# Performance work log

Hardware: AMD Instinct MI355X
Metric: run time of the kernel (lower is better)

## Reference

```python
import jax, jax.numpy as jnp
import numpy as np

B, D_IN = 4096, 32000
H0, H1, TAIL = 4000, 4000, 2000
SPARSITY = 0.98


def setup_inputs() -> dict:
    key = jax.random.key(0)
    ks = jax.random.split(key, 8)
    vals = jax.random.normal(ks[0], (B, D_IN), dtype=jnp.float32)
    mask = jax.random.uniform(ks[1], (B, D_IN)) > SPARSITY
    X = vals * mask.astype(jnp.float32)
    def xavier(k, fan_in, fan_out):
        gain = jnp.sqrt(2.0)  # calculate_gain('relu')
        bound = gain * jnp.sqrt(6.0 / (fan_in + fan_out))
        return jax.random.uniform(k, (fan_in, fan_out), dtype=jnp.float32,
                                  minval=-bound, maxval=bound)
    return {
        'X': X,
        'W_in': xavier(ks[2], D_IN, H0), 'b_in': jnp.full((H0,), 0.1, jnp.float32),
        'W1': xavier(ks[3], H0, H1),     'b1': jnp.full((H1,), 0.1, jnp.float32),
        'W2': xavier(ks[4], H1, TAIL),   'b2': jnp.full((TAIL,), 0.1, jnp.float32),
    }


def reference(X, W_in, b_in, W1, b1, W2, b2):
    # SparseLinear: sparse-dense mm + bias (here expressed as dense mm)
    out = jnp.dot(X, W_in) + b_in            # [B, H0]
    # block 0: Linear -> ReLU (dropout identity at eval)
    out = jax.nn.relu(jnp.dot(out, W1) + b1)  # [B, H1]
    # block 1 (tail): Linear -> ReLU
    out = jax.nn.relu(jnp.dot(out, W2) + b2)  # [B, TAIL]
    return out
```

## Files before the change

### kernel.cpp

```cpp
#include <hip/hip_runtime.h>
#include <stdint.h>
#include <stddef.h>


typedef __attribute__((ext_vector_type(8))) short short8;
typedef __attribute__((ext_vector_type(4))) float f32x4;
typedef __attribute__((ext_vector_type(4))) uint32_t u32x4;
typedef __attribute__((ext_vector_type(2))) uint32_t u32x2;

__device__ __forceinline__ uint32_t f2bf_bits(float f) {
  uint32_t u = __builtin_bit_cast(uint32_t, f);
  u += 0x7FFFu + ((u >> 16) & 1u);
  return u >> 16;
}
__device__ __forceinline__ uint32_t pk2(float a, float b) {
  return f2bf_bits(a) | (f2bf_bits(b) << 16);
}

__device__ __forceinline__ void gload_lds16(const uint16_t* g, uint16_t* l) {
  __builtin_amdgcn_global_load_lds(
      (const __attribute__((address_space(1))) uint32_t*)g,
      (__attribute__((address_space(3))) uint32_t*)l, 16, 0, 0);
}

__global__ __launch_bounds__(256)
void cvt_bf16_kernel(const float* __restrict__ in, uint32_t* __restrict__ out, size_t n) {
  size_t i = ((size_t)blockIdx.x * 256 + threadIdx.x) * 8;
  if (i + 8 <= n) {
    f32x4 a = *(const f32x4*)(in + i);
    f32x4 b = *(const f32x4*)(in + i + 4);
    u32x4 o = {pk2(a.x, a.y), pk2(a.z, a.w), pk2(b.x, b.y), pk2(b.z, b.w)};
    *(u32x4*)(out + i / 2) = o;
  }
}

__global__ __launch_bounds__(256)
void cvtT_bf16_kernel(const float* __restrict__ in, uint16_t* __restrict__ out, int K, int N) {
  __shared__ float tile[32][33];
  const int kb = blockIdx.y * 32;
  const int nb = blockIdx.x * 32;
  const int tx = threadIdx.x & 31;
  const int ty = threadIdx.x >> 5;
  const int ncol = nb + tx;
#pragma unroll
  for (int i = 0; i < 32; i += 8)
    tile[ty + i][tx] = (ncol < N) ? in[(size_t)(kb + ty + i) * N + ncol] : 0.f;
  __syncthreads();
#pragma unroll
  for (int i = 0; i < 32; i += 8) {
    int nrow = nb + ty + i;
    if (nrow < N)
      out[(size_t)nrow * K + (kb + tx)] = (uint16_t)f2bf_bits(tile[tx][ty + i]);
  }
}

template<bool RELU, bool OBF16>
__global__ __launch_bounds__(256, 2)
void mlp_gemm_fast(const uint16_t* __restrict__ A, const uint16_t* __restrict__ Bt,
                   const float* __restrict__ bias, void* __restrict__ Cp,
                   int M, int N, int K)
{
  __shared__ uint16_t As[128 * 32];
  __shared__ uint16_t Bs[128 * 32];

  const int tid  = threadIdx.x;
  const int lane = tid & 63;
  const int wave = __builtin_amdgcn_readfirstlane(tid >> 6);

  const int gx = gridDim.x;
  int nwg = gx * (int)gridDim.y;
  int wg = (int)blockIdx.y * gx + (int)blockIdx.x;
  if ((nwg & 7) == 0) { int c = nwg >> 3; wg = (wg & 7) * c + (wg >> 3); }
  const int n0 = (wg % gx) << 7;
  const int m0 = (wg / gx) << 7;

  const int wm = (wave & 1) << 6;
  const int wn = (wave >> 1) << 6;
  const int fl = lane & 15;
  const int kg = lane >> 4;

  const int sr = lane >> 2;
  const int sp = lane & 3;
  const int r0 = wave * 32 + sr;
  const int ssw = ((sp ^ ((r0 >> 1) & 3)) << 3);

  const uint16_t* gA0 = A + (size_t)(m0 + r0) * K + ssw;
  const uint16_t* gA1 = gA0 + (size_t)16 * K;
  int bn0 = n0 + r0;      if (bn0 > N - 1) bn0 = N - 1;
  int bn1 = n0 + r0 + 16; if (bn1 > N - 1) bn1 = N - 1;
  const uint16_t* gB0 = Bt + (size_t)bn0 * K + ssw;
  const uint16_t* gB1 = Bt + (size_t)bn1 * K + ssw;

  uint16_t* lA0 = &As[wave * 1024];
  uint16_t* lA1 = lA0 + 512;
  uint16_t* lB0 = &Bs[wave * 1024];
  uint16_t* lB1 = lB0 + 512;

  const int colsw = ((kg ^ ((fl >> 1) & 3)) << 3);

  f32x4 acc[4][4];
#pragma unroll
  for (int i = 0; i < 4; ++i)
#pragma unroll
    for (int j = 0; j < 4; ++j)
      acc[i][j] = f32x4{0.f, 0.f, 0.f, 0.f};

  for (int k0 = 0; k0 < K; k0 += 32) {
    gload_lds16(gA0, lA0);
    gload_lds16(gA1, lA1);
    gload_lds16(gB0, lB0);
    gload_lds16(gB1, lB1);
    gA0 += 32; gA1 += 32; gB0 += 32; gB1 += 32;
    __syncthreads();

    short8 af[4], bfr[4];
#pragma unroll
    for (int t = 0; t < 4; ++t) {
      af[t]  = *(const short8*)&As[(wm + t * 16 + fl) * 32 + colsw];
      bfr[t] = *(const short8*)&Bs[(wn + t * 16 + fl) * 32 + colsw];
    }
#pragma unroll
    for (int tm = 0; tm < 4; ++tm)
#pragma unroll
      for (int tn = 0; tn < 4; ++tn)
        acc[tm][tn] = __builtin_amdgcn_mfma_f32_16x16x32_bf16(af[tm], bfr[tn], acc[tm][tn], 0, 0, 0);
    __syncthreads();
  }

#pragma unroll
  for (int tn = 0; tn < 4; ++tn) {
    int n = n0 + wn + tn * 16 + fl;
    if (n < N) {
      float bv = bias[n];
#pragma unroll
      for (int tm = 0; tm < 4; ++tm) {
        size_t base = (size_t)(m0 + wm + tm * 16 + kg * 4) * N + n;
#pragma unroll
        for (int r = 0; r < 4; ++r) {
          float v = acc[tm][tn][r] + bv;
          if constexpr (RELU) v = fmaxf(v, 0.f);
          if constexpr (OBF16)
            ((uint16_t*)Cp)[base + (size_t)r * N] = (uint16_t)f2bf_bits(v);
          else
            ((float*)Cp)[base + (size_t)r * N] = v;
        }
      }
    }
  }
}

template<bool ABF16, bool BTBF16, bool RELU, bool OBF16>
__global__ __launch_bounds__(256, 2)
void mlp_gemm(const void* __restrict__ Ap, const void* __restrict__ Bp,
              const float* __restrict__ bias, void* __restrict__ Cp,
              int M, int N, int K)
{
  __shared__ uint16_t As[128][40];
  __shared__ uint16_t Bs[128][40];

  const int tid  = threadIdx.x;
  const int lane = tid & 63;
  const int wave = tid >> 6;
  const int wm = (wave & 1) << 6;
  const int wn = (wave >> 1) << 6;
  const int fl = lane & 15;
  const int kg = lane >> 4;

  const int m0 = blockIdx.y << 7;
  const int n0 = blockIdx.x << 7;

  const int ar = tid >> 1;
  const int ah = (tid & 1) << 4;
  const int bkb = tid >> 5;
  const int bnb = tid & 31;

  const bool n_full = (n0 + 128 <= N);
  const int brow = (n0 + ar < N) ? (n0 + ar) : (N - 1);

  f32x4 acc[4][4];
#pragma unroll
  for (int i = 0; i < 4; ++i)
#pragma unroll
    for (int j = 0; j < 4; ++j)
      acc[i][j] = f32x4{0.f, 0.f, 0.f, 0.f};

  for (int k0 = 0; k0 < K; k0 += 32) {
    {
      u32x4 w0, w1;
      if constexpr (ABF16) {
        const uint16_t* A = (const uint16_t*)Ap;
        const uint16_t* p = A + (size_t)(m0 + ar) * K + (k0 + ah);
        w0 = ((const u32x4*)p)[0];
        w1 = ((const u32x4*)p)[1];
      } else {
        const float* A = (const float*)Ap;
        const float* p = A + (size_t)(m0 + ar) * K + (k0 + ah);
        f32x4 a0 = ((const f32x4*)p)[0];
        f32x4 a1 = ((const f32x4*)p)[1];
        f32x4 a2 = ((const f32x4*)p)[2];
        f32x4 a3 = ((const f32x4*)p)[3];
        w0 = u32x4{pk2(a0.x, a0.y), pk2(a0.z, a0.w), pk2(a1.x, a1.y), pk2(a1.z, a1.w)};
        w1 = u32x4{pk2(a2.x, a2.y), pk2(a2.z, a2.w), pk2(a3.x, a3.y), pk2(a3.z, a3.w)};
      }
      u32x4* d = (u32x4*)&As[ar][ah];
      d[0] = w0; d[1] = w1;
    }
    if constexpr (BTBF16) {
      const uint16_t* Bt = (const uint16_t*)Bp;
      const uint16_t* p = Bt + (size_t)brow * K + (k0 + ah);
      u32x4 w0 = ((const u32x4*)p)[0];
      u32x4 w1 = ((const u32x4*)p)[1];
      u32x4* d = (u32x4*)&Bs[ar][ah];
      d[0] = w0; d[1] = w1;
    } else {
      const float* Bmat = (const float*)Bp;
      if (n_full) {
        const float* p = Bmat + (size_t)(k0 + bkb * 4) * N + (n0 + bnb * 4);
        f32x4 r0 = *(const f32x4*)p;
        f32x4 r1 = *(const f32x4*)(p + (size_t)N);
        f32x4 r2 = *(const f32x4*)(p + 2 * (size_t)N);
        f32x4 r3 = *(const f32x4*)(p + 3 * (size_t)N);
#pragma unroll
        for (int ii = 0; ii < 4; ++ii) {
          u32x2 w = {pk2(r0[ii], r1[ii]), pk2(r2[ii], r3[ii])};
          *(u32x2*)&Bs[bnb * 4 + ii][bkb * 4] = w;
        }
      } else {
#pragma unroll
        for (int ii = 0; ii < 4; ++ii) {
          int n = n0 + bnb * 4 + ii;
          uint32_t b0 = 0, b1 = 0, b2 = 0, b3 = 0;
          if (n < N) {
            size_t o = (size_t)(k0 + bkb * 4) * N + n;
            b0 = f2bf_bits(Bmat[o]);
            b1 = f2bf_bits(Bmat[o + (size_t)N]);
            b2 = f2bf_bits(Bmat[o + 2 * (size_t)N]);
            b3 = f2bf_bits(Bmat[o + 3 * (size_t)N]);
          }
          u32x2 w = {b0 | (b1 << 16), b2 | (b3 << 16)};
          *(u32x2*)&Bs[bnb * 4 + ii][bkb * 4] = w;
        }
      }
    }
    __syncthreads();

    short8 af[4], bfr[4];
#pragma unroll
    for (int t = 0; t < 4; ++t) {
      af[t]  = *(const short8*)&As[wm + t * 16 + fl][kg * 8];
      bfr[t] = *(const short8*)&Bs[wn + t * 16 + fl][kg * 8];
    }
#pragma unroll
    for (int tm = 0; tm < 4; ++tm)
#pragma unroll
      for (int tn = 0; tn < 4; ++tn)
        acc[tm][tn] = __builtin_amdgcn_mfma_f32_16x16x32_bf16(af[tm], bfr[tn], acc[tm][tn], 0, 0, 0);
    __syncthreads();
  }

#pragma unroll
  for (int tn = 0; tn < 4; ++tn) {
    int n = n0 + wn + tn * 16 + fl;
    if (n < N) {
      float bv = bias[n];
#pragma unroll
      for (int tm = 0; tm < 4; ++tm) {
        size_t base = (size_t)(m0 + wm + tm * 16 + kg * 4) * N + n;
#pragma unroll
        for (int r = 0; r < 4; ++r) {
          float v = acc[tm][tn][r] + bv;
          if constexpr (RELU) v = fmaxf(v, 0.f);
          if constexpr (OBF16)
            ((uint16_t*)Cp)[base + (size_t)r * N] = (uint16_t)f2bf_bits(v);
          else
            ((float*)Cp)[base + (size_t)r * N] = v;
        }
      }
    }
  }
}

extern "C" void kernel_launch(void* const* d_in, const int* in_sizes, int n_in,
                              void* d_out, int out_size, void* d_ws, size_t ws_size,
                              hipStream_t stream) {
  const float* X   = (const float*)d_in[0];
  const float* Win = (const float*)d_in[1];
  const float* bin = (const float*)d_in[2];
  const float* W1  = (const float*)d_in[3];
  const float* b1  = (const float*)d_in[4];
  const float* W2  = (const float*)d_in[5];
  const float* b2  = (const float*)d_in[6];
  float* out = (float*)d_out;

  const int Bm = 4096, DIN = 32000, H0 = 4000, H1 = 4000, TL = 2000;
  const size_t sX  = (size_t)Bm * DIN;
  const size_t sWi = (size_t)DIN * H0;
  const size_t sW1 = (size_t)H0 * H1;
  const size_t sW2 = (size_t)H1 * TL;
  const size_t st0 = (size_t)Bm * H0;
  const size_t st1 = (size_t)Bm * H1;
  const size_t need_fast = 2 * (sX + sWi + sW1 + sW2 + st0 + st1);

  dim3 blk(256);

  if (ws_size >= need_fast) {
    uint8_t* w = (uint8_t*)d_ws;
    uint16_t* Xb  = (uint16_t*)w; w += 2 * sX;
    uint16_t* WiT = (uint16_t*)w; w += 2 * sWi;
    uint16_t* W1T = (uint16_t*)w; w += 2 * sW1;
    uint16_t* W2T = (uint16_t*)w; w += 2 * sW2;
    uint16_t* t0  = (uint16_t*)w; w += 2 * st0;
    uint16_t* t1  = (uint16_t*)w;

    cvt_bf16_kernel<<<dim3((unsigned)((sX / 8 + 255) / 256)), blk, 0, stream>>>(X, (uint32_t*)Xb, sX);
    cvtT_bf16_kernel<<<dim3((H0 + 31) / 32, DIN / 32), blk, 0, stream>>>(Win, WiT, DIN, H0);
    cvtT_bf16_kernel<<<dim3((H1 + 31) / 32, H0 / 32), blk, 0, stream>>>(W1, W1T, H0, H1);
    cvtT_bf16_kernel<<<dim3((TL + 31) / 32, H1 / 32), blk, 0, stream>>>(W2, W2T, H1, TL);

    mlp_gemm_fast<false, true><<<dim3((H0 + 127) / 128, Bm / 128), blk, 0, stream>>>(
        Xb, WiT, bin, t0, Bm, H0, DIN);
    mlp_gemm_fast<true, true><<<dim3((H1 + 127) / 128, Bm / 128), blk, 0, stream>>>(
        t0, W1T, b1, t1, Bm, H1, H0);
    mlp_gemm_fast<true, false><<<dim3((TL + 127) / 128, Bm / 128), blk, 0, stream>>>(
        t1, W2T, b2, out, Bm, TL, H1);
  } else {
    uint16_t* t0 = (uint16_t*)d_ws;
    uint16_t* t1 = t0 + st0;

    mlp_gemm<false, false, false, true><<<dim3((H0 + 127) / 128, Bm / 128), blk, 0, stream>>>(
        X, Win, bin, t0, Bm, H0, DIN);
    mlp_gemm<true, false, true, true><<<dim3((H1 + 127) / 128, Bm / 128), blk, 0, stream>>>(
        t0, W1, b1, t1, Bm, H1, H0);
    mlp_gemm<true, false, true, false><<<dim3((TL + 127) / 128, Bm / 128), blk, 0, stream>>>(
        t1, W2, b2, out, Bm, TL, H1);
  }
}
```

Measured before the change: 3.128 ms.

## Double-buffer LDS tiles to overlap global loads with MFMA compute

Adds a second LDS buffer for the A and B tiles so the next K-tile is prefetched via global_load_lds while MFMAs run on the current one. Explicit vmcnt waits and raw s_barrier calls replace __syncthreads, with sched_barrier fences to keep the compiler from reordering across them. The intent is to hide global-memory latency in the GEMM main loop. It doubles LDS use, which may reduce occupancy under launch_bounds(256,2), and relies on exact vmcnt counting being correct.

```diff
diff --git a/kernel.cpp b/kernel.cpp
--- a/kernel.cpp
+++ b/kernel.cpp
@@ -60,8 +60,8 @@
                    const float* __restrict__ bias, void* __restrict__ Cp,
                    int M, int N, int K)
 {
-  __shared__ uint16_t As[128 * 32];
-  __shared__ uint16_t Bs[128 * 32];
+  __shared__ uint16_t As[2][128 * 32];
+  __shared__ uint16_t Bs[2][128 * 32];
 
   const int tid  = threadIdx.x;
   const int lane = tid & 63;
@@ -91,10 +91,7 @@
   const uint16_t* gB0 = Bt + (size_t)bn0 * K + ssw;
   const uint16_t* gB1 = Bt + (size_t)bn1 * K + ssw;
 
-  uint16_t* lA0 = &As[wave * 1024];
-  uint16_t* lA1 = lA0 + 512;
-  uint16_t* lB0 = &Bs[wave * 1024];
-  uint16_t* lB1 = lB0 + 512;
+  const int lofs = wave * 1024;
 
   const int colsw = ((kg ^ ((fl >> 1) & 3)) << 3);
 
@@ -105,26 +102,46 @@
     for (int j = 0; j < 4; ++j)
       acc[i][j] = f32x4{0.f, 0.f, 0.f, 0.f};
 
-  for (int k0 = 0; k0 < K; k0 += 32) {
-    gload_lds16(gA0, lA0);
-    gload_lds16(gA1, lA1);
-    gload_lds16(gB0, lB0);
-    gload_lds16(gB1, lB1);
+  auto stage = [&](int buf) {
+    uint16_t* a = &As[buf][lofs];
+    uint16_t* b = &Bs[buf][lofs];
+    gload_lds16(gA0, a);
+    gload_lds16(gA1, a + 512);
+    gload_lds16(gB0, b);
+    gload_lds16(gB1, b + 512);
     gA0 += 32; gA1 += 32; gB0 += 32; gB1 += 32;
-    __syncthreads();
-
+  };
+
+  const int nt = K >> 5;
+  stage(0);
+
+  for (int t = 0; t < nt; ++t) {
+    const int cur = t & 1;
+    if (t + 1 < nt) {
+      stage(cur ^ 1);
+      asm volatile("s_waitcnt vmcnt(4)" ::: "memory");
+    } else {
+      asm volatile("s_waitcnt vmcnt(0)" ::: "memory");
+    }
+    __builtin_amdgcn_s_barrier();
+    __builtin_amdgcn_sched_barrier(0);
+
+    const uint16_t* Asr = As[cur];
+    const uint16_t* Bsr = Bs[cur];
     short8 af[4], bfr[4];
 #pragma unroll
-    for (int t = 0; t < 4; ++t) {
-      af[t]  = *(const short8*)&As[(wm + t * 16 + fl) * 32 + colsw];
-      bfr[t] = *(const short8*)&Bs[(wn + t * 16 + fl) * 32 + colsw];
+    for (int q = 0; q < 4; ++q) {
+      af[q]  = *(const short8*)&Asr[(wm + q * 16 + fl) * 32 + colsw];
+      bfr[q] = *(const short8*)&Bsr[(wn + q * 16 + fl) * 32 + colsw];
     }
 #pragma unroll
     for (int tm = 0; tm < 4; ++tm)
 #pragma unroll
       for (int tn = 0; tn < 4; ++tn)
         acc[tm][tn] = __builtin_amdgcn_mfma_f32_16x16x32_bf16(af[tm], bfr[tn], acc[tm][tn], 0, 0, 0);
-    __syncthreads();
+
+    __builtin_amdgcn_sched_barrier(0);
+    __builtin_amdgcn_s_barrier();
   }
 
 #pragma unroll
```

Result: no change. 3.118 ms (-0.3%).
